# Kernel tuning notes

Measured on AMD Instinct MI355X. Metric: run time of the kernel, lower is better.

## Reference

```python
import jax, jax.numpy as jnp
import numpy as np
from jax import lax

# Dimensions (see shape_source)
B, J, I, E, H = 256, 128, 64, 512, 512   # batch, target len, source len, embed, hidden
MAXJW = 128                               # max jump width
WJ = 2 * MAXJW + 1                        # size of jump-width set (257)
ALPHA_P0 = 1.0
EPS = 1e-29


def setup_inputs() -> dict:
    key = jax.random.key(0)
    ks = jax.random.split(key, 10)
    return {
        "y_hidden": jax.random.normal(ks[0], (B, J, E), jnp.float32),
        "y_hidden_null": jax.random.normal(ks[1], (1, 1, E), jnp.float32),
        "W_trans": jax.random.normal(ks[2], (E, H), jnp.float32) * 0.02,
        "b_trans": jnp.zeros((H,), jnp.float32),
        "W_jump": jax.random.normal(ks[3], (H, WJ), jnp.float32) * 0.02,
        "b_jump": jnp.zeros((WJ,), jnp.float32),
        "W_p0": jax.random.normal(ks[4], (H, 1), jnp.float32) * 0.02,
        "b_p0": jnp.zeros((1,), jnp.float32),
        # emission probs p(source_t | target_state_k), kept near 1 to avoid
        # underflow of the unrescaled HMM forward product (as in original).
        "emission": jax.random.uniform(ks[5], (B, 2 * J, I), jnp.float32) * 0.5 + 0.75,
        "source_lengths": jax.random.randint(ks[6], (B,), 1, I + 1, dtype=jnp.int32),
        "target_lengths": jax.random.randint(ks[7], (B,), 1, J + 1, dtype=jnp.int32),
    }


def _build_transition(y_hidden, y_hidden_null, W_trans, b_trans, W_jump, b_jump, W_p0, b_p0):
    # get_transition: Dense(tanh) -> Dense(softmax) jump widths; Dense(sigmoid) p0.
    ts = jnp.tanh(y_hidden @ W_trans + b_trans)           # [B,J,H]
    ts_null = jnp.tanh(y_hidden_null @ W_trans + b_trans) # [1,1,H]
    jump_prob = jax.nn.softmax(ts @ W_jump + b_jump, axis=-1)  # [B,J,WJ]
    p0_scalar = ALPHA_P0 * jax.nn.sigmoid(ts_null @ W_p0 + b_p0)[0, 0, 0]
    p0 = jnp.broadcast_to(p0_scalar, (y_hidden.shape[0], J))  # tile to [B,J]
    # gather jump widths: row i takes jump_prob[:, i, MAXJW + k - i] for k in [0,J)
    idx = MAXJW + jnp.arange(J)[None, :] - jnp.arange(J)[:, None]        # [J,J]
    idxb = jnp.broadcast_to(idx[None], (jump_prob.shape[0], J, J))
    jw = jnp.take_along_axis(jump_prob, idxb, axis=2)                    # [B,J,J]
    jw = jw * (1.0 - p0[:, :, None]) / jnp.sum(jw, axis=2, keepdims=True)
    diag_p0 = p0[:, :, None] * jnp.eye(J, dtype=jw.dtype)                # [B,J,J]
    T_half = jnp.concatenate([jw, diag_p0], axis=2)                      # [B,J,2J]
    return jnp.concatenate([T_half, T_half], axis=1)                     # [B,2J,2J]


def reference(y_hidden, y_hidden_null, W_trans, b_trans, W_jump, b_jump,
              W_p0, b_p0, emission, source_lengths, target_lengths):
    T = _build_transition(y_hidden, y_hidden_null, W_trans, b_trans,
                          W_jump, b_jump, W_p0, b_p0)       # [B,2J,2J]
    e = jnp.transpose(emission, (2, 0, 1))                  # [I,B,2J]
    # tf.scan with no initializer: f_0 = emission at source position 0
    f0 = e[0]

    def step(f, et):
        f_next = jnp.einsum('bj,bjk->bk', f, T) * et        # forward recursion
        return f_next, f_next

    _, fs = lax.scan(step, f0, e[1:])
    fs = jnp.concatenate([f0[None], fs], axis=0)            # [I,B,2J]
    fbt = jnp.transpose(fs, (1, 2, 0))                      # [B,2J,I]
    last_idx = (source_lengths - 1).astype(jnp.int32)[:, None, None]
    last = jnp.take_along_axis(fbt, last_idx, axis=2)[:, :, 0]  # [B,2J]
    m = (jnp.arange(J)[None, :] < target_lengths[:, None]).astype(last.dtype)
    mask = jnp.concatenate([m, m], axis=1)                  # [B,2J]
    return jnp.log(jnp.sum(last * mask, axis=1) + EPS)      # [B]
```

## Files before the change

kernel.cpp:

```cpp
#include <hip/hip_runtime.h>
#include <stdint.h>

typedef __attribute__((ext_vector_type(8))) short bf16x8;
typedef __attribute__((ext_vector_type(4))) float f32x4;

__device__ __forceinline__ unsigned short f2bf(float f) {
  union { float f; unsigned int u; } un; un.f = f;
  unsigned int r = un.u + 0x7fffu + ((un.u >> 16) & 1u);
  return (unsigned short)(r >> 16);
}

__device__ __forceinline__ float tanh_fast(float x) {
  x = fminf(15.f, fmaxf(-15.f, x));
  float e = __expf(2.f * x);
  return (e - 1.f) / (e + 1.f);
}

__device__ __forceinline__ unsigned int cvt_pk_bf16(float lo, float hi) {
  unsigned int r;
  asm("v_cvt_pk_bf16_f32 %0, %1, %2" : "=v"(r) : "v"(lo), "v"(hi));
  return r;
}

__device__ __forceinline__ void gload_lds16(const void* g, void* l) {
  __builtin_amdgcn_global_load_lds(
      (const __attribute__((address_space(1))) unsigned int*)(unsigned long long)g,
      (__attribute__((address_space(3))) unsigned int*)(unsigned int)(unsigned long long)l,
      16, 0, 0);
}

__global__ __launch_bounds__(256) void cvt_weights_p0(
    const float* __restrict__ Wt_in, const float* __restrict__ Wj_in,
    const float* __restrict__ ynull, const float* __restrict__ b_trans,
    const float* __restrict__ W_p0, const float* __restrict__ b_p0,
    unsigned short* __restrict__ wt, unsigned short* __restrict__ wj,
    float* __restrict__ p0buf) {
  if (blockIdx.x < 1536) {
    const int i = blockIdx.x * 256 + threadIdx.x;
    if (i < 512 * 512) {
      const int c = i >> 9, r = i & 511;
      wt[i] = f2bf(Wt_in[(size_t)r * 512 + c]);
    } else {
      const int j = i - 512 * 512;
      const int c = j >> 9, r = j & 511;
      wj[j] = f2bf(Wj_in[(size_t)r * 257 + c]);
    }
    return;
  }
  __shared__ float red[256];
  const int hh = threadIdx.x;
  float a0 = 0.f, a1 = 0.f;
  for (int e = 0; e < 512; ++e) {
    const float y = ynull[e];
    a0 = fmaf(y, Wt_in[(size_t)e * 512 + hh], a0);
    a1 = fmaf(y, Wt_in[(size_t)e * 512 + hh + 256], a1);
  }
  red[hh] = tanhf(a0 + b_trans[hh]) * W_p0[hh] +
            tanhf(a1 + b_trans[hh + 256]) * W_p0[hh + 256];
  __syncthreads();
  for (int s = 128; s > 0; s >>= 1) {
    if (hh < s) red[hh] += red[hh + s];
    __syncthreads();
  }
  if (hh == 0) {
    const float z = red[0] + b_p0[0];
    const float p0 = 1.f / (1.f + __expf(-z));
    p0buf[0] = p0;
    p0buf[1] = 1.f - p0;
  }
}


__global__ __launch_bounds__(256, 2) void gemm_af32(
    const float* __restrict__ A, const unsigned short* __restrict__ Bt,
    const float* __restrict__ bias, unsigned short* __restrict__ Cout,
    int M, int N, int K) {
  __shared__ unsigned short sA[128 * 32];
  __shared__ unsigned short sB[256 * 32];
  const int tid = threadIdx.x;
  const int lane = tid & 63;
  const int wave = tid >> 6;
  const int wr = wave >> 1, wc = wave & 1;
  const int m0 = blockIdx.x * 128, n0 = blockIdx.y * 256;

  f32x4 acc[4][8] = {};

  const int srow = lane >> 2;
  const int sl = lane & 3;
  const int scol = sl * 8;
  const int wsz = (srow >> 1) & 3;
  const int scolw = (sl ^ wsz) * 8;
  const int c0 = wave * 2, c1 = wave * 2 + 1;
  const float* Af0 = A + (size_t)(m0 + c0 * 16 + srow) * K + scol;
  const float* Af1 = A + (size_t)(m0 + c1 * 16 + srow) * K + scol;

  float4 a00 = *reinterpret_cast<const float4*>(Af0);
  float4 a01 = *reinterpret_cast<const float4*>(Af0 + 4);
  float4 a10 = *reinterpret_cast<const float4*>(Af1);
  float4 a11 = *reinterpret_cast<const float4*>(Af1 + 4);

  const int r15 = lane & 15;
  const int oslot = ((lane >> 4) ^ ((r15 >> 1) & 3)) * 8;

  for (int kk = 0; kk < K; kk += 32) {
    __syncthreads();
    {
      union { unsigned int u[4]; bf16x8 v; } p;
      p.u[0] = cvt_pk_bf16(a00.x, a00.y);
      p.u[1] = cvt_pk_bf16(a00.z, a00.w);
      p.u[2] = cvt_pk_bf16(a01.x, a01.y);
      p.u[3] = cvt_pk_bf16(a01.z, a01.w);
      *reinterpret_cast<bf16x8*>(&sA[c0 * 512 + srow * 32 + scolw]) = p.v;
      p.u[0] = cvt_pk_bf16(a10.x, a10.y);
      p.u[1] = cvt_pk_bf16(a10.z, a10.w);
      p.u[2] = cvt_pk_bf16(a11.x, a11.y);
      p.u[3] = cvt_pk_bf16(a11.z, a11.w);
      *reinterpret_cast<bf16x8*>(&sA[c1 * 512 + srow * 32 + scolw]) = p.v;
    }
#pragma unroll
    for (int j = 0; j < 4; ++j) {
      const int c = wave * 4 + j;
      gload_lds16(Bt + (size_t)(n0 + c * 16 + srow) * K + kk + scolw,
                  &sB[c * 512]);
    }
    __syncthreads();
    if (kk + 32 < K) {
      a00 = *reinterpret_cast<const float4*>(Af0 + kk + 32);
      a01 = *reinterpret_cast<const float4*>(Af0 + kk + 36);
      a10 = *reinterpret_cast<const float4*>(Af1 + kk + 32);
      a11 = *reinterpret_cast<const float4*>(Af1 + kk + 36);
    }
    bf16x8 af[4], bfr[8];
#pragma unroll
    for (int mi = 0; mi < 4; ++mi)
      af[mi] = *reinterpret_cast<const bf16x8*>(
          &sA[(wr * 64 + mi * 16 + r15) * 32 + oslot]);
#pragma unroll
    for (int ni = 0; ni < 8; ++ni)
      bfr[ni] = *reinterpret_cast<const bf16x8*>(
          &sB[(wc * 128 + ni * 16 + r15) * 32 + oslot]);
#pragma unroll
    for (int mi = 0; mi < 4; ++mi)
#pragma unroll
      for (int ni = 0; ni < 8; ++ni)
        acc[mi][ni] = __builtin_amdgcn_mfma_f32_16x16x32_bf16(
            af[mi], bfr[ni], acc[mi][ni], 0, 0, 0);
  }

  const int crow0 = m0 + wr * 64 + (lane >> 4) * 4;
  const int ccol0 = n0 + wc * 128 + r15;
#pragma unroll
  for (int mi = 0; mi < 4; ++mi) {
#pragma unroll
    for (int ni = 0; ni < 8; ++ni) {
      const int gcol = ccol0 + ni * 16;
      const float bv = bias[gcol];
#pragma unroll
      for (int r = 0; r < 4; ++r) {
        const int grow = crow0 + mi * 16 + r;
        Cout[(size_t)grow * N + gcol] = f2bf(tanh_fast(acc[mi][ni][r] + bv));
      }
    }
  }
}

#define LG_STRIDE 260
__global__ __launch_bounds__(256, 2) void gemm2_sm(
    const unsigned short* __restrict__ A,
    const unsigned short* __restrict__ Bt,
    const float* __restrict__ bias,
    const float* __restrict__ p0buf,
    unsigned short* __restrict__ jwout) {
  __shared__ __align__(16) char smem[64 * LG_STRIDE * 4];
  const int tid = threadIdx.x;
  const int lane = tid & 63;
  const int wave = tid >> 6;
  const int m0 = blockIdx.x * 64;
  const int r15 = lane & 15;
  const int q = lane >> 4;
  const int wr = wave >> 1, wc = wave & 1;

  f32x4 acc[2][8] = {};

  const int srow = lane >> 2;
  const int sl = lane & 3;
  const int scolw = ((sl ^ ((srow >> 1) & 3))) * 8;
  const int oslot = ((q ^ ((r15 >> 1) & 3))) * 8;

  auto stage = [&](int bi, int t) {
    unsigned short* base = (unsigned short*)(smem + bi * 20480);
#pragma unroll
    for (int cc = 0; cc < 5; ++cc) {
      const int chunk = wave + cc * 4;
      if (chunk < 4) {
        gload_lds16(A + (size_t)(m0 + chunk * 16 + srow) * 512 + t * 32 + scolw,
                    base + chunk * 512);
      } else {
        gload_lds16(Bt + (size_t)((chunk - 4) * 16 + srow) * 512 + t * 32 + scolw,
                    base + 2048 + (chunk - 4) * 512);
      }
    }
  };
  auto compute = [&](int bi) {
    const unsigned short* base = (const unsigned short*)(smem + bi * 20480);
    bf16x8 af[2], bfr[8];
#pragma unroll
    for (int mi = 0; mi < 2; ++mi)
      af[mi] = *reinterpret_cast<const bf16x8*>(
          &base[(wr * 32 + mi * 16 + r15) * 32 + oslot]);
#pragma unroll
    for (int ni = 0; ni < 8; ++ni)
      bfr[ni] = *reinterpret_cast<const bf16x8*>(
          &base[2048 + (wc * 128 + ni * 16 + r15) * 32 + oslot]);
#pragma unroll
    for (int mi = 0; mi < 2; ++mi)
#pragma unroll
      for (int ni = 0; ni < 8; ++ni)
        acc[mi][ni] = __builtin_amdgcn_mfma_f32_16x16x32_bf16(
            af[mi], bfr[ni], acc[mi][ni], 0, 0, 0);
  };

  stage(0, 0);
  __syncthreads();
  for (int t = 0; t < 16; ++t) {
    if (t + 1 < 16) stage((t + 1) & 1, t + 1);
    compute(t & 1);
    __syncthreads();
  }

  float* lg = (float*)smem;
#pragma unroll
  for (int mi = 0; mi < 2; ++mi) {
#pragma unroll
    for (int ni = 0; ni < 8; ++ni) {
      const int col = wc * 128 + ni * 16 + r15;
      const float bv = bias[col];
#pragma unroll
      for (int r = 0; r < 4; ++r) {
        const int rowL = wr * 32 + mi * 16 + q * 4 + r;
        lg[rowL * LG_STRIDE + col] = acc[mi][ni][r] + bv;
      }
    }
  }
  __syncthreads();

  const int rowL = tid >> 2, p = tid & 3;
  const int grow = m0 + rowL;
  const int i = grow & 127;
  float* lrow = lg + rowL * LG_STRIDE + (128 - i) + p * 32;
  float mx = -1e30f;
#pragma unroll
  for (int j = 0; j < 32; ++j) mx = fmaxf(mx, lrow[j]);
  mx = fmaxf(mx, __shfl_xor(mx, 1));
  mx = fmaxf(mx, __shfl_xor(mx, 2));
  float s = 0.f;
#pragma unroll
  for (int j = 0; j < 32; ++j) {
    const float e = __expf(lrow[j] - mx);
    lrow[j] = e;
    s += e;
  }
  s += __shfl_xor(s, 1);
  s += __shfl_xor(s, 2);
  const float scale = p0buf[1] / s;
  unsigned int* orow = (unsigned int*)(jwout + (size_t)grow * 128 + p * 32);
#pragma unroll
  for (int j = 0; j < 16; ++j)
    orow[j] = cvt_pk_bf16(lrow[2 * j] * scale, lrow[2 * j + 1] * scale);
}

#define SE_STRIDE 264
__global__ __launch_bounds__(256, 1) void forward_fused(
    const unsigned short* __restrict__ jwb,
    const float* __restrict__ emission,
    const float* __restrict__ p0buf, const int* __restrict__ slen_p,
    const int* __restrict__ tlen_p, float* __restrict__ out) {
  __shared__ __align__(16) float se[64 * SE_STRIDE];
  __shared__ __align__(16) unsigned short gl16[128];
  const int b = blockIdx.x;
  const int tid = threadIdx.x;
  const float* eb = emission + (size_t)b * 16384;

  bf16x8 bfr[4][8];
  const int l = tid & 63;
  const int m = l & 15;
  const int q = l >> 4;

  if (tid >= 64) {
#pragma unroll
    for (int it = 0; it < 6; ++it) {
      const int tau = (tid - 64) + 192 * it;
      if (tau < 1024) {
        const int t0 = (tau & 15) * 4;
        const int mm = (tau >> 4) & 15;
        const int nt0 = ((tau >> 8) & 1) * 4;
        const int half = (tau >> 9) & 1;
        const int kbase = half * 128 + nt0 * 16 + mm;
        const float4 v0 = *reinterpret_cast<const float4*>(&eb[(size_t)(kbase) * 64 + t0]);
        const float4 v1 = *reinterpret_cast<const float4*>(&eb[(size_t)(kbase + 16) * 64 + t0]);
        const float4 v2 = *reinterpret_cast<const float4*>(&eb[(size_t)(kbase + 32) * 64 + t0]);
        const float4 v3 = *reinterpret_cast<const float4*>(&eb[(size_t)(kbase + 48) * 64 + t0]);
        const int jinv0 = half * 128 + mm * 8 + nt0;
        float* d = &se[(size_t)t0 * SE_STRIDE + jinv0];
        *reinterpret_cast<float4*>(d) = (float4){v0.x, v1.x, v2.x, v3.x};
        *reinterpret_cast<float4*>(d + SE_STRIDE) = (float4){v0.y, v1.y, v2.y, v3.y};
        *reinterpret_cast<float4*>(d + 2 * SE_STRIDE) = (float4){v0.z, v1.z, v2.z, v3.z};
        *reinterpret_cast<float4*>(d + 3 * SE_STRIDE) = (float4){v0.w, v1.w, v2.w, v3.w};
      }
    }
  } else {
    const unsigned short* jwt = jwb + (size_t)b * 16384;
#pragma unroll
    for (int kt = 0; kt < 4; ++kt) {
      const int r0 = kt * 32 + q * 8;
#pragma unroll
      for (int nt = 0; nt < 8; ++nt) {
        const int c = nt * 16 + m;
        bf16x8 v;
#pragma unroll
        for (int j = 0; j < 8; ++j) v[j] = (short)jwt[(size_t)(r0 + j) * 128 + c];
        bfr[kt][nt] = v;
      }
    }
  }
  __syncthreads();
  if (tid >= 64) return;

  const float p0 = p0buf[0];
  const int S = slen_p[b];
  const int T = tlen_p[b];

  float gown[8];
  {
    const float4 i0a = *reinterpret_cast<const float4*>(&se[m * 8]);
    const float4 i0b = *reinterpret_cast<const float4*>(&se[m * 8 + 4]);
    const float4 i1a = *reinterpret_cast<const float4*>(&se[128 + m * 8]);
    const float4 i1b = *reinterpret_cast<const float4*>(&se[128 + m * 8 + 4]);
    gown[0] = i0a.x + i1a.x; gown[1] = i0a.y + i1a.y;
    gown[2] = i0a.z + i1a.z; gown[3] = i0a.w + i1a.w;
    gown[4] = i0b.x + i1b.x; gown[5] = i0b.y + i1b.y;
    gown[6] = i0b.z + i1b.z; gown[7] = i0b.w + i1b.w;
  }
  gl16[(2 * q) * 16 + m]     = f2bf(gown[2 * q]);
  gl16[(2 * q + 1) * 16 + m] = f2bf(gown[2 * q + 1]);

  for (int t = 1; t < S; ++t) {
    const float* st = &se[(size_t)t * SE_STRIDE];
    const float4 pe0a = *reinterpret_cast<const float4*>(&st[m * 8]);
    const float4 pe0b = *reinterpret_cast<const float4*>(&st[m * 8 + 4]);
    const float4 pe1a = *reinterpret_cast<const float4*>(&st[128 + m * 8]);
    const float4 pe1b = *reinterpret_cast<const float4*>(&st[128 + m * 8 + 4]);
    const float e0[8] = {pe0a.x, pe0a.y, pe0a.z, pe0a.w, pe0b.x, pe0b.y, pe0b.z, pe0b.w};
    const float e1[8] = {pe1a.x, pe1a.y, pe1a.z, pe1a.w, pe1b.x, pe1b.y, pe1b.z, pe1b.w};
    float h[8];
#pragma unroll
    for (int nt = 0; nt < 8; ++nt) h[nt] = gown[nt] * (p0 * e1[nt]);
    bf16x8 af[4];
#pragma unroll
    for (int kt = 0; kt < 4; ++kt)
      af[kt] = *reinterpret_cast<const bf16x8*>(&gl16[kt * 32 + q * 8]);
    f32x4 acc[8];
#pragma unroll
    for (int nt = 0; nt < 8; ++nt) {
      f32x4 a = __builtin_amdgcn_mfma_f32_16x16x32_bf16(
          af[0], bfr[0][nt], (f32x4){0.f, 0.f, 0.f, 0.f}, 0, 0, 0);
      a = __builtin_amdgcn_mfma_f32_16x16x32_bf16(af[1], bfr[1][nt], a, 0, 0, 0);
      a = __builtin_amdgcn_mfma_f32_16x16x32_bf16(af[2], bfr[2][nt], a, 0, 0, 0);
      acc[nt] = __builtin_amdgcn_mfma_f32_16x16x32_bf16(af[3], bfr[3][nt], a, 0, 0, 0);
    }
#pragma unroll
    for (int nt = 0; nt < 8; ++nt) gown[nt] = fmaf(acc[nt][0], e0[nt], h[nt]);
    gl16[(2 * q) * 16 + m]     = f2bf(gown[2 * q]);
    gl16[(2 * q + 1) * 16 + m] = f2bf(gown[2 * q + 1]);
  }

  float val = 0.f;
#pragma unroll
  for (int nt = 0; nt < 8; ++nt)
    if (nt * 16 + m < T) val += gown[nt];
#pragma unroll
  for (int off = 1; off < 16; off <<= 1) val += __shfl_xor(val, off);
  if (l == 0) out[b] = logf(val + 1e-29f);
}

extern "C" void kernel_launch(void* const* d_in, const int* in_sizes, int n_in,
                              void* d_out, int out_size, void* d_ws, size_t ws_size,
                              hipStream_t stream) {
  const float* y_hidden = (const float*)d_in[0];
  const float* y_null   = (const float*)d_in[1];
  const float* W_trans  = (const float*)d_in[2];
  const float* b_trans  = (const float*)d_in[3];
  const float* W_jump   = (const float*)d_in[4];
  const float* b_jump   = (const float*)d_in[5];
  const float* W_p0     = (const float*)d_in[6];
  const float* b_p0     = (const float*)d_in[7];
  const float* emission = (const float*)d_in[8];
  const int* slen = (const int*)d_in[9];
  const int* tlen = (const int*)d_in[10];
  float* out = (float*)d_out;

  char* ws = (char*)d_ws;
  unsigned short* ts16  = (unsigned short*)ws;
  unsigned short* wt16t = (unsigned short*)(ws + 50331648);
  unsigned short* wj16t = (unsigned short*)(ws + 50855936);
  float* p0buf          = (float*)(ws + 51118080);
  unsigned short* jwb16 = (unsigned short*)(ws + 51118336);

  cvt_weights_p0<<<dim3(1537), dim3(256), 0, stream>>>(
      W_trans, W_jump, y_null, b_trans, W_p0, b_p0, wt16t, wj16t, p0buf);

  gemm_af32<<<dim3(256, 2), dim3(256), 0, stream>>>(y_hidden, wt16t, b_trans, ts16,
                                                    32768, 512, 512);
  gemm2_sm<<<dim3(512), dim3(256), 0, stream>>>(ts16, wj16t, b_jump, p0buf, jwb16);
  forward_fused<<<dim3(256), dim3(256), 0, stream>>>(jwb16, emission, p0buf,
                                                     slen, tlen, out);
}
```

Measured before the change: 110.5 us.

## Load GEMM B operand straight from global and drop block-wide syncs

The first GEMM (tanh projection) no longer stages the bf16 weight tile in shared memory. Each wave now reads its B fragments directly from global memory into registers. Each wave also owns a private 32-row slice of the A tile in LDS, so both __syncthreads per k-step are removed. The N tile shrinks from 256 to 128, doubling the grid in N, so the fp32 activation matrix A is read twice as often, and B loads are issued in the same iteration they are consumed, so their latency may be exposed.

```diff
diff --git a/kernel.cpp b/kernel.cpp
--- a/kernel.cpp
+++ b/kernel.cpp
@@ -76,34 +76,32 @@
     const float* __restrict__ bias, unsigned short* __restrict__ Cout,
     int M, int N, int K) {
   __shared__ unsigned short sA[128 * 32];
-  __shared__ unsigned short sB[256 * 32];
   const int tid = threadIdx.x;
   const int lane = tid & 63;
-  const int wave = tid >> 6;
-  const int wr = wave >> 1, wc = wave & 1;
-  const int m0 = blockIdx.x * 128, n0 = blockIdx.y * 256;
-
-  f32x4 acc[4][8] = {};
+  const int w = tid >> 6;
+  const int m0 = blockIdx.x * 128, n0 = blockIdx.y * 128;
+  const int r15 = lane & 15;
+  const int q = lane >> 4;
+
+  f32x4 acc[2][8] = {};
 
   const int srow = lane >> 2;
   const int sl = lane & 3;
   const int scol = sl * 8;
-  const int wsz = (srow >> 1) & 3;
-  const int scolw = (sl ^ wsz) * 8;
-  const int c0 = wave * 2, c1 = wave * 2 + 1;
+  const int scolw = (sl ^ ((srow >> 1) & 3)) * 8;
+  const int c0 = w * 2, c1 = w * 2 + 1;
   const float* Af0 = A + (size_t)(m0 + c0 * 16 + srow) * K + scol;
   const float* Af1 = A + (size_t)(m0 + c1 * 16 + srow) * K + scol;
+  const unsigned short* Brow = Bt + (size_t)(n0 + r15) * K + q * 8;
 
   float4 a00 = *reinterpret_cast<const float4*>(Af0);
   float4 a01 = *reinterpret_cast<const float4*>(Af0 + 4);
   float4 a10 = *reinterpret_cast<const float4*>(Af1);
   float4 a11 = *reinterpret_cast<const float4*>(Af1 + 4);
 
-  const int r15 = lane & 15;
-  const int oslot = ((lane >> 4) ^ ((r15 >> 1) & 3)) * 8;
+  const int oslot = (q ^ ((r15 >> 1) & 3)) * 8;
 
   for (int kk = 0; kk < K; kk += 32) {
-    __syncthreads();
     {
       union { unsigned int u[4]; bf16x8 v; } p;
       p.u[0] = cvt_pk_bf16(a00.x, a00.y);
@@ -117,48 +115,40 @@
       p.u[3] = cvt_pk_bf16(a11.z, a11.w);
       *reinterpret_cast<bf16x8*>(&sA[c1 * 512 + srow * 32 + scolw]) = p.v;
     }
-#pragma unroll
-    for (int j = 0; j < 4; ++j) {
-      const int c = wave * 4 + j;
-      gload_lds16(Bt + (size_t)(n0 + c * 16 + srow) * K + kk + scolw,
-                  &sB[c * 512]);
-    }
-    __syncthreads();
     if (kk + 32 < K) {
       a00 = *reinterpret_cast<const float4*>(Af0 + kk + 32);
       a01 = *reinterpret_cast<const float4*>(Af0 + kk + 36);
       a10 = *reinterpret_cast<const float4*>(Af1 + kk + 32);
       a11 = *reinterpret_cast<const float4*>(Af1 + kk + 36);
     }
-    bf16x8 af[4], bfr[8];
-#pragma unroll
-    for (int mi = 0; mi < 4; ++mi)
-      af[mi] = *reinterpret_cast<const bf16x8*>(
-          &sA[(wr * 64 + mi * 16 + r15) * 32 + oslot]);
+    bf16x8 bfr[8];
 #pragma unroll
     for (int ni = 0; ni < 8; ++ni)
       bfr[ni] = *reinterpret_cast<const bf16x8*>(
-          &sB[(wc * 128 + ni * 16 + r15) * 32 + oslot]);
-#pragma unroll
-    for (int mi = 0; mi < 4; ++mi)
+          Brow + (size_t)ni * 16 * K + kk);
+    bf16x8 af[2];
+#pragma unroll
+    for (int mi = 0; mi < 2; ++mi)
+      af[mi] = *reinterpret_cast<const bf16x8*>(
+          &sA[(w * 32 + mi * 16 + r15) * 32 + oslot]);
+#pragma unroll
+    for (int mi = 0; mi < 2; ++mi)
 #pragma unroll
       for (int ni = 0; ni < 8; ++ni)
         acc[mi][ni] = __builtin_amdgcn_mfma_f32_16x16x32_bf16(
             af[mi], bfr[ni], acc[mi][ni], 0, 0, 0);
   }
 
-  const int crow0 = m0 + wr * 64 + (lane >> 4) * 4;
-  const int ccol0 = n0 + wc * 128 + r15;
-#pragma unroll
-  for (int mi = 0; mi < 4; ++mi) {
+#pragma unroll
+  for (int mi = 0; mi < 2; ++mi) {
+    const int crow0 = m0 + w * 32 + mi * 16 + q * 4;
 #pragma unroll
     for (int ni = 0; ni < 8; ++ni) {
-      const int gcol = ccol0 + ni * 16;
+      const int gcol = n0 + ni * 16 + r15;
       const float bv = bias[gcol];
 #pragma unroll
       for (int r = 0; r < 4; ++r) {
-        const int grow = crow0 + mi * 16 + r;
-        Cout[(size_t)grow * N + gcol] = f2bf(tanh_fast(acc[mi][ni][r] + bv));
+        Cout[(size_t)(crow0 + r) * N + gcol] = f2bf(tanh_fast(acc[mi][ni][r] + bv));
       }
     }
   }
@@ -409,7 +399,7 @@
   cvt_weights_p0<<<dim3(1537), dim3(256), 0, stream>>>(
       W_trans, W_jump, y_null, b_trans, W_p0, b_p0, wt16t, wj16t, p0buf);
 
-  gemm_af32<<<dim3(256, 2), dim3(256), 0, stream>>>(y_hidden, wt16t, b_trans, ts16,
+  gemm_af32<<<dim3(256, 4), dim3(256), 0, stream>>>(y_hidden, wt16t, b_trans, ts16,
                                                     32768, 512, 512);
   gemm2_sm<<<dim3(512), dim3(256), 0, stream>>>(ts16, wj16t, b_jump, p0buf, jwb16);
   forward_fused<<<dim3(256), dim3(256), 0, stream>>>(jwb16, emission, p0buf,
```

Measured after the change: 154.8 us. 1.4x slower.
